# Performance work log

Hardware: AMD Instinct MI355X
Metric: run time of the kernel (lower is better)

## Reference

```python
import jax, jax.numpy as jnp
import numpy as np

TAU = 2.0       # LIF membrane time constant
V_TH = 1.0      # spike threshold
ALPHA = 2.0     # ATan surrogate sharpness
EPS = 1e-5      # BatchNorm eps


@jax.custom_vjp
def spike_fn(x):
    return (x >= 0.0).astype(x.dtype)

def _spike_fwd(x):
    return spike_fn(x), x

def _spike_bwd(x, g):
    # ATan surrogate: alpha/2 / (1 + (pi/2 * alpha * x)^2)
    sg = (ALPHA / 2.0) / (1.0 + (jnp.pi / 2.0 * ALPHA * x) ** 2)
    return (g * sg,)

spike_fn.defvjp(_spike_fwd, _spike_bwd)


def lif_multistep(x):
    # x: [T, B, C, L]; spikingjelly LIFNode, decay_input=True, hard reset to 0,
    # detach_reset=True (spike detached in the reset path only).
    def step(v, xt):
        v = v + (xt - v) / TAU
        s = spike_fn(v - V_TH)
        v = (1.0 - jax.lax.stop_gradient(s)) * v
        return v, s
    v0 = jnp.zeros_like(x[0])
    _, spks = jax.lax.scan(step, v0, x)
    return spks  # [T, B, C, L]


def delta_encoder(inputs, bn_gamma, bn_beta, enc_w, enc_b):
    # inputs: [B, L, C]
    delta = jnp.concatenate(
        [jnp.zeros_like(inputs[:, :1]), inputs[:, 1:] - inputs[:, :-1]], axis=1
    )  # [B, L, C]
    d = jnp.transpose(delta, (0, 2, 1))[:, None]  # [B, 1, C, L]
    # BatchNorm2d(1), training mode: stats over all elements (single channel)
    mean = jnp.mean(d)
    var = jnp.var(d)
    d = (d - mean) * jax.lax.rsqrt(var + EPS) * bn_gamma[0] + bn_beta[0]
    d = jnp.transpose(d, (0, 2, 3, 1))  # [B, C, L, 1]
    # Linear(1, T): enc[b,c,l,t] = d[b,c,l,0] * w[t,0] + b[t]
    enc = d * enc_w[:, 0] + enc_b  # [B, C, L, T]
    enc = jnp.transpose(enc, (3, 0, 1, 2))  # [T, B, C, L]
    spks = lif_multistep(enc)
    return jnp.transpose(spks, (1, 0, 2, 3))  # [B, T, C, L]


def setup_inputs() -> dict:
    key = jax.random.key(0)
    k1, k2, k3 = jax.random.split(key, 3)
    B, L, C, T = 32, 4096, 8, 64
    inputs = jax.random.normal(k1, (B, L, C), dtype=jnp.float32)
    bn_gamma = jnp.ones((1,), dtype=jnp.float32)
    bn_beta = jnp.zeros((1,), dtype=jnp.float32)
    # torch Linear(1, T) init: U(-1, 1) since fan_in = 1
    enc_w = jax.random.uniform(k2, (T, 1), dtype=jnp.float32, minval=-1.0, maxval=1.0)
    enc_b = jax.random.uniform(k3, (T,), dtype=jnp.float32, minval=-1.0, maxval=1.0)
    return {"inputs": inputs, "bn_gamma": bn_gamma, "bn_beta": bn_beta,
            "enc_w": enc_w, "enc_b": enc_b}


def reference(inputs, bn_gamma, bn_beta, enc_w, enc_b):
    return delta_encoder(inputs, bn_gamma, bn_beta, enc_w, enc_b)
```

## Files before the change

### kernel.cpp

```cpp
#include <hip/hip_runtime.h>
#include <math.h>

#define NBATCH 32
#define NL     4096
#define NC     8
#define NT     64
#define NTOT   (NBATCH * NL * NC)

typedef float f32x4 __attribute__((ext_vector_type(4)));

__global__ __launch_bounds__(256) void reduce_kernel(const float* __restrict__ in,
                                                     double* __restrict__ part) {
    __shared__ double sm[256], sm2[256];
    const int tid = threadIdx.x;
    const f32x4* in4 = reinterpret_cast<const f32x4*>(in);
    double s = 0.0, s2 = 0.0;
    for (int g = blockIdx.x * 256 + tid; g < NTOT / 4; g += 256 * 256) {
        const int e = g * 4;
        if ((e & (NL * NC - 1)) >= NC) {
            const f32x4 cur = in4[g];
            const f32x4 prv = in4[g - 2];
            const double d0 = (double)cur.x - (double)prv.x;
            const double d1 = (double)cur.y - (double)prv.y;
            const double d2 = (double)cur.z - (double)prv.z;
            const double d3 = (double)cur.w - (double)prv.w;
            s  += d0 + d1 + d2 + d3;
            s2 += d0 * d0 + d1 * d1 + d2 * d2 + d3 * d3;
        }
    }
    sm[tid] = s; sm2[tid] = s2;
    __syncthreads();
    for (int off = 128; off > 0; off >>= 1) {
        if (tid < off) { sm[tid] += sm[tid + off]; sm2[tid] += sm2[tid + off]; }
        __syncthreads();
    }
    if (tid == 0) {
        part[2 * blockIdx.x]     = sm[0];
        part[2 * blockIdx.x + 1] = sm2[0];
    }
}

__global__ __launch_bounds__(256) void finalize_kernel(const double* __restrict__ part,
                                                       const float* __restrict__ gamma,
                                                       const float* __restrict__ beta,
                                                       const float* __restrict__ wv,
                                                       const float* __restrict__ bv,
                                                       double2* __restrict__ pq) {
    __shared__ double sm[256], sm2[256];
    __shared__ double sAB[2];
    const int tid = threadIdx.x;
    sm[tid]  = part[2 * tid];
    sm2[tid] = part[2 * tid + 1];
    __syncthreads();
    for (int off = 128; off > 0; off >>= 1) {
        if (tid < off) { sm[tid] += sm[tid + off]; sm2[tid] += sm2[tid + off]; }
        __syncthreads();
    }
    if (tid == 0) {
        const double mean = sm[0] / (double)NTOT;
        const double var  = sm2[0] / (double)NTOT - mean * mean;
        const double inv  = 1.0 / sqrt(var + 1e-5);
        const double A    = inv * (double)gamma[0];
        const double Bc   = (double)beta[0] - mean * A;
        sAB[0] = A;
        sAB[1] = Bc;
    }
    __syncthreads();
    if (tid < NT) {
        const double A  = sAB[0];
        const double Bc = sAB[1];
        const double w  = (double)wv[tid];
        const double b  = (double)bv[tid];
        double2 r;
        r.x = 0.5 * A * w;
        r.y = 0.5 * (Bc * w + b);
        pq[tid] = r;
    }
}

__global__ __launch_bounds__(256) void lif_kernel(const float* __restrict__ in,
                                                  const double2* __restrict__ pq,
                                                  float* __restrict__ out) {
    __shared__ __align__(16) double2 spq[NT];
    const int tid = threadIdx.x;
    if (tid < NT) spq[tid] = pq[tid];
    __syncthreads();

    const int blk   = blockIdx.x;
    const int chunk = blk & 7;
    const int bc    = blk >> 3;
    const int c     = bc & 7;
    const int b     = bc >> 3;
    const int l     = chunk * 512 + tid * 2;

    const float* base = in + (b * NL + l) * NC + c;
    const float p0 = (l == 0) ? 0.0f : base[-NC];
    const float c0 = base[0];
    const float c1 = base[NC];

    const double dl0 = (l == 0) ? 0.0 : ((double)c0 - (double)p0);
    const double dl1 = (double)c1 - (double)c0;

    double v0 = 0.0, v1 = 0.0;
    float2* obase = reinterpret_cast<float2*>(out + ((b * NT) * NC + c) * NL + l);

#pragma unroll 8
    for (int t = 0; t < NT; t++) {
        const double2 PQ = spq[t];
        float2 o;
        double vv;
        bool s;

        vv = fma(v0, 0.5, fma(dl0, PQ.x, PQ.y));
        s = vv >= 1.0; o.x = s ? 1.0f : 0.0f; v0 = s ? 0.0 : vv;

        vv = fma(v1, 0.5, fma(dl1, PQ.x, PQ.y));
        s = vv >= 1.0; o.y = s ? 1.0f : 0.0f; v1 = s ? 0.0 : vv;

        obase[t * (NC * NL / 2)] = o;
    }
}

extern "C" void kernel_launch(void* const* d_in, const int* in_sizes, int n_in,
                              void* d_out, int out_size, void* d_ws, size_t ws_size,
                              hipStream_t stream) {
    const float* inputs = (const float*)d_in[0];
    const float* gamma  = (const float*)d_in[1];
    const float* beta   = (const float*)d_in[2];
    const float* enc_w  = (const float*)d_in[3];
    const float* enc_b  = (const float*)d_in[4];
    float* out = (float*)d_out;

    double*  part = (double*)d_ws;
    double2* pq   = (double2*)(part + 512);

    reduce_kernel  <<<256,  256, 0, stream>>>(inputs, part);
    finalize_kernel<<<1,    256, 0, stream>>>(part, gamma, beta, enc_w, enc_b, pq);
    lif_kernel     <<<2048, 256, 0, stream>>>(inputs, pq, out);
}
```

Before: 274.5 us.

## Process four positions per thread and batch spike stores via bitmasks

The LIF kernel now gives each thread four consecutive L positions instead of two, launched as 512 blocks of 512 threads. It writes float4 stores instead of float2. The time loop is split into two halves of 32 steps: spikes are first computed into per-lane bitmasks, then written out in a separate loop. This separates the dependent fp64 recurrence from the stores and widens memory transactions. The cost is fewer threads and blocks overall (lower parallelism on a 256-CU part) and more registers per thread.

```diff
diff --git a/kernel.cpp b/kernel.cpp
--- a/kernel.cpp
+++ b/kernel.cpp
@@ -78,7 +78,7 @@
     }
 }
 
-__global__ __launch_bounds__(256) void lif_kernel(const float* __restrict__ in,
+__global__ __launch_bounds__(512) void lif_kernel(const float* __restrict__ in,
                                                   const double2* __restrict__ pq,
                                                   float* __restrict__ out) {
     __shared__ __align__(16) double2 spq[NT];
@@ -86,38 +86,69 @@
     if (tid < NT) spq[tid] = pq[tid];
     __syncthreads();
 
-    const int blk   = blockIdx.x;
-    const int chunk = blk & 7;
-    const int bc    = blk >> 3;
-    const int c     = bc & 7;
-    const int b     = bc >> 3;
-    const int l     = chunk * 512 + tid * 2;
+    const int blk  = blockIdx.x;
+    const int half = blk & 1;
+    const int c    = (blk >> 1) & 7;
+    const int b    = blk >> 4;
+    const int l    = half * 2048 + tid * 4;
 
     const float* base = in + (b * NL + l) * NC + c;
-    const float p0 = (l == 0) ? 0.0f : base[-NC];
-    const float c0 = base[0];
-    const float c1 = base[NC];
+    const float xm = (l == 0) ? 0.0f : base[-NC];
+    const float x0 = base[0];
+    const float x1 = base[NC];
+    const float x2 = base[2 * NC];
+    const float x3 = base[3 * NC];
 
-    const double dl0 = (l == 0) ? 0.0 : ((double)c0 - (double)p0);
-    const double dl1 = (double)c1 - (double)c0;
+    const double d0 = (l == 0) ? 0.0 : ((double)x0 - (double)xm);
+    const double d1 = (double)x1 - (double)x0;
+    const double d2 = (double)x2 - (double)x1;
+    const double d3 = (double)x3 - (double)x2;
 
-    double v0 = 0.0, v1 = 0.0;
-    float2* obase = reinterpret_cast<float2*>(out + ((b * NT) * NC + c) * NL + l);
+    double v0 = 0.0, v1 = 0.0, v2 = 0.0, v3 = 0.0;
+
+    float4* op = reinterpret_cast<float4*>(out + ((b * NT) * NC + c) * NL + l);
+    const int tstride = NC * NL / 4;
+
+    unsigned mA0 = 0, mA1 = 0, mA2 = 0, mA3 = 0;
+#pragma unroll 8
+    for (int t = 0; t < 32; ++t) {
+        const double2 PQ = spq[t];
+        double vv; bool s;
+        vv = fma(v0, 0.5, fma(d0, PQ.x, PQ.y)); s = vv >= 1.0; mA0 = mA0 + mA0 + (s ? 1u : 0u); v0 = s ? 0.0 : vv;
+        vv = fma(v1, 0.5, fma(d1, PQ.x, PQ.y)); s = vv >= 1.0; mA1 = mA1 + mA1 + (s ? 1u : 0u); v1 = s ? 0.0 : vv;
+        vv = fma(v2, 0.5, fma(d2, PQ.x, PQ.y)); s = vv >= 1.0; mA2 = mA2 + mA2 + (s ? 1u : 0u); v2 = s ? 0.0 : vv;
+        vv = fma(v3, 0.5, fma(d3, PQ.x, PQ.y)); s = vv >= 1.0; mA3 = mA3 + mA3 + (s ? 1u : 0u); v3 = s ? 0.0 : vv;
+    }
 
 #pragma unroll 8
-    for (int t = 0; t < NT; t++) {
+    for (int t = 0; t < 32; ++t) {
+        float4 o;
+        o.x = ((int)mA0 < 0) ? 1.0f : 0.0f; mA0 <<= 1;
+        o.y = ((int)mA1 < 0) ? 1.0f : 0.0f; mA1 <<= 1;
+        o.z = ((int)mA2 < 0) ? 1.0f : 0.0f; mA2 <<= 1;
+        o.w = ((int)mA3 < 0) ? 1.0f : 0.0f; mA3 <<= 1;
+        op[t * tstride] = o;
+    }
+
+    unsigned mB0 = 0, mB1 = 0, mB2 = 0, mB3 = 0;
+#pragma unroll 8
+    for (int t = 32; t < 64; ++t) {
         const double2 PQ = spq[t];
-        float2 o;
-        double vv;
-        bool s;
+        double vv; bool s;
+        vv = fma(v0, 0.5, fma(d0, PQ.x, PQ.y)); s = vv >= 1.0; mB0 = mB0 + mB0 + (s ? 1u : 0u); v0 = s ? 0.0 : vv;
+        vv = fma(v1, 0.5, fma(d1, PQ.x, PQ.y)); s = vv >= 1.0; mB1 = mB1 + mB1 + (s ? 1u : 0u); v1 = s ? 0.0 : vv;
+        vv = fma(v2, 0.5, fma(d2, PQ.x, PQ.y)); s = vv >= 1.0; mB2 = mB2 + mB2 + (s ? 1u : 0u); v2 = s ? 0.0 : vv;
+        vv = fma(v3, 0.5, fma(d3, PQ.x, PQ.y)); s = vv >= 1.0; mB3 = mB3 + mB3 + (s ? 1u : 0u); v3 = s ? 0.0 : vv;
+    }
 
-        vv = fma(v0, 0.5, fma(dl0, PQ.x, PQ.y));
-        s = vv >= 1.0; o.x = s ? 1.0f : 0.0f; v0 = s ? 0.0 : vv;
-
-        vv = fma(v1, 0.5, fma(dl1, PQ.x, PQ.y));
-        s = vv >= 1.0; o.y = s ? 1.0f : 0.0f; v1 = s ? 0.0 : vv;
-
-        obase[t * (NC * NL / 2)] = o;
+#pragma unroll 8
+    for (int t = 32; t < 64; ++t) {
+        float4 o;
+        o.x = ((int)mB0 < 0) ? 1.0f : 0.0f; mB0 <<= 1;
+        o.y = ((int)mB1 < 0) ? 1.0f : 0.0f; mB1 <<= 1;
+        o.z = ((int)mB2 < 0) ? 1.0f : 0.0f; mB2 <<= 1;
+        o.w = ((int)mB3 < 0) ? 1.0f : 0.0f; mB3 <<= 1;
+        op[t * tstride] = o;
     }
 }
 
@@ -134,7 +165,7 @@
     double*  part = (double*)d_ws;
     double2* pq   = (double2*)(part + 512);
 
-    reduce_kernel  <<<256,  256, 0, stream>>>(inputs, part);
-    finalize_kernel<<<1,    256, 0, stream>>>(part, gamma, beta, enc_w, enc_b, pq);
-    lif_kernel     <<<2048, 256, 0, stream>>>(inputs, pq, out);
+    reduce_kernel  <<<256, 256, 0, stream>>>(inputs, part);
+    finalize_kernel<<<1,   256, 0, stream>>>(part, gamma, beta, enc_w, enc_b, pq);
+    lif_kernel     <<<512, 512, 0, stream>>>(inputs, pq, out);
 }
```

Result: slower. 281.0 us (+2.3%).

## Fuse reduction, finalize and LIF into one kernel with grid-wide atomic barrier

Applied to the files above, without the earlier changes.

Merges the three kernels into a single persistent-style kernel. Each of 256 blocks of 1024 threads computes its slice's delta statistics, atomically accumulates them globally, spins on a counter until all blocks arrive, then computes BN/encoder coefficients and runs the LIF recurrence. Each thread now handles four L positions and writes float4. This removes two launches and the re-read of the input, but relies on all 256 blocks being co-resident (deadlock risk otherwise), adds a memset, and makes the FP64 sum order nondeterministic.

```diff
diff --git a/kernel.cpp b/kernel.cpp
--- a/kernel.cpp
+++ b/kernel.cpp
@@ -6,118 +6,92 @@
 #define NC     8
 #define NT     64
 #define NTOT   (NBATCH * NL * NC)
+#define NBLK   256
 
-typedef float f32x4 __attribute__((ext_vector_type(4)));
+__global__ __launch_bounds__(1024) void fused_kernel(const float* __restrict__ in,
+                                                     const float* __restrict__ gamma,
+                                                     const float* __restrict__ beta,
+                                                     const float* __restrict__ wv,
+                                                     const float* __restrict__ bv,
+                                                     double* __restrict__ acc,
+                                                     unsigned* __restrict__ cnt,
+                                                     float* __restrict__ out) {
+    __shared__ double sm[1024], sm2[1024];
+    __shared__ __align__(16) double2 spq[NT];
+    __shared__ double sAB[2];
 
-__global__ __launch_bounds__(256) void reduce_kernel(const float* __restrict__ in,
-                                                     double* __restrict__ part) {
-    __shared__ double sm[256], sm2[256];
     const int tid = threadIdx.x;
-    const f32x4* in4 = reinterpret_cast<const f32x4*>(in);
-    double s = 0.0, s2 = 0.0;
-    for (int g = blockIdx.x * 256 + tid; g < NTOT / 4; g += 256 * 256) {
-        const int e = g * 4;
-        if ((e & (NL * NC - 1)) >= NC) {
-            const f32x4 cur = in4[g];
-            const f32x4 prv = in4[g - 2];
-            const double d0 = (double)cur.x - (double)prv.x;
-            const double d1 = (double)cur.y - (double)prv.y;
-            const double d2 = (double)cur.z - (double)prv.z;
-            const double d3 = (double)cur.w - (double)prv.w;
-            s  += d0 + d1 + d2 + d3;
-            s2 += d0 * d0 + d1 * d1 + d2 * d2 + d3 * d3;
-        }
-    }
-    sm[tid] = s; sm2[tid] = s2;
+    const int blk = blockIdx.x;
+    const int c   = blk & 7;
+    const int b   = blk >> 3;
+    const int l   = tid * 4;
+
+    const float* base = in + (b * NL + l) * NC + c;
+    const float xm = (l == 0) ? 0.0f : base[-NC];
+    const float x0 = base[0];
+    const float x1 = base[NC];
+    const float x2 = base[2 * NC];
+    const float x3 = base[3 * NC];
+
+    const double d0 = (l == 0) ? 0.0 : ((double)x0 - (double)xm);
+    const double d1 = (double)x1 - (double)x0;
+    const double d2 = (double)x2 - (double)x1;
+    const double d3 = (double)x3 - (double)x2;
+
+    sm[tid]  = d0 + d1 + d2 + d3;
+    sm2[tid] = d0 * d0 + d1 * d1 + d2 * d2 + d3 * d3;
     __syncthreads();
-    for (int off = 128; off > 0; off >>= 1) {
+    for (int off = 512; off > 0; off >>= 1) {
         if (tid < off) { sm[tid] += sm[tid + off]; sm2[tid] += sm2[tid + off]; }
         __syncthreads();
     }
+
     if (tid == 0) {
-        part[2 * blockIdx.x]     = sm[0];
-        part[2 * blockIdx.x + 1] = sm2[0];
-    }
-}
-
-__global__ __launch_bounds__(256) void finalize_kernel(const double* __restrict__ part,
-                                                       const float* __restrict__ gamma,
-                                                       const float* __restrict__ beta,
-                                                       const float* __restrict__ wv,
-                                                       const float* __restrict__ bv,
-                                                       double2* __restrict__ pq) {
-    __shared__ double sm[256], sm2[256];
-    __shared__ double sAB[2];
-    const int tid = threadIdx.x;
-    sm[tid]  = part[2 * tid];
-    sm2[tid] = part[2 * tid + 1];
-    __syncthreads();
-    for (int off = 128; off > 0; off >>= 1) {
-        if (tid < off) { sm[tid] += sm[tid + off]; sm2[tid] += sm2[tid + off]; }
-        __syncthreads();
-    }
-    if (tid == 0) {
-        const double mean = sm[0] / (double)NTOT;
-        const double var  = sm2[0] / (double)NTOT - mean * mean;
+        __hip_atomic_fetch_add(&acc[0], sm[0],  __ATOMIC_RELAXED, __HIP_MEMORY_SCOPE_AGENT);
+        __hip_atomic_fetch_add(&acc[1], sm2[0], __ATOMIC_RELAXED, __HIP_MEMORY_SCOPE_AGENT);
+        __hip_atomic_fetch_add(cnt, 1u, __ATOMIC_ACQ_REL, __HIP_MEMORY_SCOPE_AGENT);
+        unsigned v;
+        do {
+            __builtin_amdgcn_s_sleep(2);
+            v = __hip_atomic_load(cnt, __ATOMIC_ACQUIRE, __HIP_MEMORY_SCOPE_AGENT);
+        } while (v < NBLK);
+        const double S    = __hip_atomic_load(&acc[0], __ATOMIC_RELAXED, __HIP_MEMORY_SCOPE_AGENT);
+        const double S2   = __hip_atomic_load(&acc[1], __ATOMIC_RELAXED, __HIP_MEMORY_SCOPE_AGENT);
+        const double mean = S / (double)NTOT;
+        const double var  = S2 / (double)NTOT - mean * mean;
         const double inv  = 1.0 / sqrt(var + 1e-5);
         const double A    = inv * (double)gamma[0];
-        const double Bc   = (double)beta[0] - mean * A;
         sAB[0] = A;
-        sAB[1] = Bc;
+        sAB[1] = (double)beta[0] - mean * A;
     }
     __syncthreads();
     if (tid < NT) {
         const double A  = sAB[0];
         const double Bc = sAB[1];
         const double w  = (double)wv[tid];
-        const double b  = (double)bv[tid];
+        const double bb = (double)bv[tid];
         double2 r;
         r.x = 0.5 * A * w;
-        r.y = 0.5 * (Bc * w + b);
-        pq[tid] = r;
+        r.y = 0.5 * (Bc * w + bb);
+        spq[tid] = r;
     }
-}
-
-__global__ __launch_bounds__(256) void lif_kernel(const float* __restrict__ in,
-                                                  const double2* __restrict__ pq,
-                                                  float* __restrict__ out) {
-    __shared__ __align__(16) double2 spq[NT];
-    const int tid = threadIdx.x;
-    if (tid < NT) spq[tid] = pq[tid];
     __syncthreads();
 
-    const int blk   = blockIdx.x;
-    const int chunk = blk & 7;
-    const int bc    = blk >> 3;
-    const int c     = bc & 7;
-    const int b     = bc >> 3;
-    const int l     = chunk * 512 + tid * 2;
-
-    const float* base = in + (b * NL + l) * NC + c;
-    const float p0 = (l == 0) ? 0.0f : base[-NC];
-    const float c0 = base[0];
-    const float c1 = base[NC];
-
-    const double dl0 = (l == 0) ? 0.0 : ((double)c0 - (double)p0);
-    const double dl1 = (double)c1 - (double)c0;
-
-    double v0 = 0.0, v1 = 0.0;
-    float2* obase = reinterpret_cast<float2*>(out + ((b * NT) * NC + c) * NL + l);
+    double v0 = 0.0, v1 = 0.0, v2 = 0.0, v3 = 0.0;
+    float4* op = reinterpret_cast<float4*>(out + ((b * NT) * NC + c) * NL + l);
+    const int tstride = NC * NL / 4;
 
 #pragma unroll 8
-    for (int t = 0; t < NT; t++) {
+    for (int t = 0; t < NT; ++t) {
         const double2 PQ = spq[t];
-        float2 o;
+        float4 o;
         double vv;
         bool s;
-
-        vv = fma(v0, 0.5, fma(dl0, PQ.x, PQ.y));
-        s = vv >= 1.0; o.x = s ? 1.0f : 0.0f; v0 = s ? 0.0 : vv;
-
-        vv = fma(v1, 0.5, fma(dl1, PQ.x, PQ.y));
-        s = vv >= 1.0; o.y = s ? 1.0f : 0.0f; v1 = s ? 0.0 : vv;
-
-        obase[t * (NC * NL / 2)] = o;
+        vv = fma(v0, 0.5, fma(d0, PQ.x, PQ.y)); s = vv >= 1.0; o.x = s ? 1.0f : 0.0f; v0 = s ? 0.0 : vv;
+        vv = fma(v1, 0.5, fma(d1, PQ.x, PQ.y)); s = vv >= 1.0; o.y = s ? 1.0f : 0.0f; v1 = s ? 0.0 : vv;
+        vv = fma(v2, 0.5, fma(d2, PQ.x, PQ.y)); s = vv >= 1.0; o.z = s ? 1.0f : 0.0f; v2 = s ? 0.0 : vv;
+        vv = fma(v3, 0.5, fma(d3, PQ.x, PQ.y)); s = vv >= 1.0; o.w = s ? 1.0f : 0.0f; v3 = s ? 0.0 : vv;
+        op[t * tstride] = o;
     }
 }
 
@@ -131,10 +105,11 @@
     const float* enc_b  = (const float*)d_in[4];
     float* out = (float*)d_out;
 
-    double*  part = (double*)d_ws;
-    double2* pq   = (double2*)(part + 512);
+    double*   acc = (double*)d_ws;
+    unsigned* cnt = (unsigned*)((char*)d_ws + 16);
 
-    reduce_kernel  <<<256,  256, 0, stream>>>(inputs, part);
-    finalize_kernel<<<1,    256, 0, stream>>>(part, gamma, beta, enc_w, enc_b, pq);
-    lif_kernel     <<<2048, 256, 0, stream>>>(inputs, pq, out);
+    hipMemsetAsync(d_ws, 0, 32, stream);
+
+    fused_kernel<<<NBLK, 1024, 0, stream>>>(inputs, gamma, beta, enc_w, enc_b,
+                                            acc, cnt, out);
 }
```

Result: slower. 299.4 us (+9.0%).
